# Performance work log

Measured on AMD Instinct MI355X. Metric: run time of the kernel, lower is better.

The kernel has to match this reference:

```python
import jax, jax.numpy as jnp
import numpy as np

B, IN, NC, O, H = 256, 2048, 1000, 4096, 4  # batch, in_features, num_classes, n_decoders, hidden
NEG_SLOPE = 0.1

def setup_inputs() -> dict:
    key = jax.random.key(0)
    ks = jax.random.split(key, 7)
    s1 = 1.0 / np.sqrt(IN)
    s2 = 1.0 / np.sqrt(H)
    return {
        "x":   jax.random.normal(ks[0], (B, IN), jnp.float32),
        "fcW": jax.random.normal(ks[1], (NC, IN), jnp.float32) * s1,
        "fcb": jax.random.normal(ks[2], (NC,), jnp.float32) * s1,
        "W1":  jax.random.normal(ks[3], (O, IN, H), jnp.float32) * s1,
        "b1":  jax.random.normal(ks[4], (O, H), jnp.float32) * s1,
        "W2":  jax.random.normal(ks[5], (O, H), jnp.float32) * s2,
        "b2":  jax.random.normal(ks[6], (O,), jnp.float32) * s2,
    }

def reference(x, fcW, fcb, W1, b1, W2, b2):
    # fc head: x1 = x @ fcW^T + fcb  -> [B, NC]
    x1 = jnp.einsum("bi,ci->bc", x, fcW) + fcb
    # 4096 tiny MLPs batched into one grouped GEMM:
    # h = leaky_relu(x @ W1_o + b1_o) for each decoder o  -> [B, O, H]
    h = jnp.einsum("bi,oih->boh", x, W1) + b1
    h = jnp.where(h >= 0, h, NEG_SLOPE * h)
    # second layer (H->1) collapses to a weighted reduction -> [B, O]
    x2 = jnp.einsum("boh,oh->bo", h, W2) + b2
    return (x1, x2)
```

## Files before the change

kernel.cpp:

```cpp
#include <hip/hip_runtime.h>


typedef __bf16 bf16_t;
typedef __bf16 bf16x8 __attribute__((ext_vector_type(8)));
typedef float  f32x4  __attribute__((ext_vector_type(4)));
typedef float  f32x16 __attribute__((ext_vector_type(16)));

#define GLDS(gp, lp) __builtin_amdgcn_global_load_lds( \
    (const __attribute__((address_space(1))) void*)(gp), \
    (__attribute__((address_space(3))) void*)(lp), 16, 0, 0)

#define WS_A_OFF 0
#define WS_F_OFF (64 * 16384)

__global__ __launch_bounds__(256)
void pack_tiles(const float* __restrict__ x, const float* __restrict__ fcW,
                char* __restrict__ ws)
{
    const int tid = threadIdx.x;
    const int bid = blockIdx.x;
    if (bid < 64) {
        const int rg = bid >> 5, kt = bid & 31;
        char* dst = ws + WS_A_OFF + (size_t)bid * 16384;
        #pragma unroll
        for (int i = 0; i < 4; ++i) {
            const int gi = tid + 256 * i;
            const int r = gi >> 3, s = gi & 7, g = s ^ (r & 7);
            const float* sp = x + (size_t)(rg * 128 + r) * 2048 + kt * 64 + g * 8;
            f32x4 v0 = *(const f32x4*)sp, v1 = *(const f32x4*)(sp + 4);
            bf16x8 o;
            #pragma unroll
            for (int c = 0; c < 4; ++c) { o[c] = (bf16_t)v0[c]; o[4 + c] = (bf16_t)v1[c]; }
            *(bf16x8*)(dst + r * 128 + s * 16) = o;
        }
    } else {
        const int t = bid - 64;
        const int cg = t >> 5, kt = t & 31;
        char* dst = ws + WS_F_OFF + (size_t)t * 8192;
        #pragma unroll
        for (int i = 0; i < 2; ++i) {
            const int gi = tid + 256 * i;
            const int n = gi >> 3, s = gi & 7, g = s ^ (n & 7);
            const int c = cg * 64 + n;
            bf16x8 o;
            if (c < 1000) {
                const float* sp = fcW + (size_t)c * 2048 + kt * 64 + g * 8;
                f32x4 v0 = *(const f32x4*)sp, v1 = *(const f32x4*)(sp + 4);
                #pragma unroll
                for (int cc = 0; cc < 4; ++cc) { o[cc] = (bf16_t)v0[cc]; o[4 + cc] = (bf16_t)v1[cc]; }
            } else {
                #pragma unroll
                for (int cc = 0; cc < 8; ++cc) o[cc] = (bf16_t)0.f;
            }
            *(bf16x8*)(dst + n * 128 + s * 16) = o;
        }
    }
}

__global__ __launch_bounds__(256, 1)
void fused_dual(const char* __restrict__ ws,
                const float* __restrict__ W1,
                const float* __restrict__ fcb,
                const float* __restrict__ b1,
                const float* __restrict__ W2,
                const float* __restrict__ b2,
                float* __restrict__ out)
{
    __shared__ __align__(16) char lds[131072];
    char* lB = lds;

    const int tid  = threadIdx.x;
    const int lane = tid & 63, w = tid >> 6;
    const int l31  = lane & 31, half = lane >> 5;

    const int idx = blockIdx.x;
    const int wid = (idx < 512) ? ((idx & 7) * 64 + (idx >> 3)) : idx;
    const bool is_fc = (wid >= 512);
    const int d   = wid;
    const int fcI = wid - 512;

    const int o_loc = tid & 7;
    const float* w1o = W1 + (size_t)(d * 8 + o_loc) * 8192;
    const int cbase = (tid >> 3) * 4;

    const int cgo = fcI >> 1, rowhalf = fcI & 1;
    const char* fcSrc = ws + WS_F_OFF + (size_t)cgo * 32 * 8192 + rowhalf * 4096;

    f32x4 rga[8], rgb[8];
    auto BL = [&](int kh, int r, f32x4* R) {
        const float* p = w1o + kh * 4096 + (cbase + r) * 32;
        #pragma unroll
        for (int j = 0; j < 8; ++j) R[j] = *(const f32x4*)(p + j * 4);
    };
    auto BW = [&](int r, const f32x4* R) {
        const int idxk = cbase + r;
        const int ktl = idxk >> 3, g = idxk & 7;
        char* base = lB + ktl * 4096 + (4 * o_loc) * 128;
        #pragma unroll
        for (int h = 0; h < 4; ++h) {
            bf16x8 v;
            #pragma unroll
            for (int j = 0; j < 8; ++j) v[j] = (bf16_t)R[j][h];
            const int n7 = (4 * o_loc + h) & 7;
            *(bf16x8*)(base + h * 128 + ((g ^ n7) << 4)) = v;
        }
    };

    auto GLDS_A = [&](int ktg, int pbuf) {
        char* dst = lds + 65536 + pbuf * 32768 + w * 8192;
        const char* src = ws + WS_A_OFF + (size_t)(w >> 1) * 524288
                        + (size_t)ktg * 16384 + (w & 1) * 8192 + lane * 16;
        #pragma unroll
        for (int i = 0; i < 8; ++i)
            GLDS(src + i * 1024, dst + i * 1024);
    };

    f32x16 acc[2];
    #pragma unroll
    for (int i = 0; i < 2; ++i)
        #pragma unroll
        for (int r = 0; r < 16; ++r) acc[i][r] = 0.f;

    for (int kh = 0; kh < 2; ++kh) {
        if (is_fc) {
            #pragma unroll
            for (int ktl = 0; ktl < 16; ++ktl)
                GLDS(fcSrc + (size_t)(kh * 16 + ktl) * 8192 + w * 1024 + lane * 16,
                     lB + ktl * 4096 + w * 1024);
        } else {
            BL(kh, 0, rga); BL(kh, 1, rgb);
            BW(0, rga);     BL(kh, 2, rga);
            BW(1, rgb);     BL(kh, 3, rgb);
            BW(2, rga);     BW(3, rgb);
        }
        GLDS_A(kh * 16, 0);
        __syncthreads();

        for (int ktl = 0; ktl < 16; ++ktl) {
            const int p = ktl & 1;
            if (ktl < 15) GLDS_A(kh * 16 + ktl + 1, p ^ 1);
            const char* A  = lds + 65536 + p * 32768;
            const char* Bt = lB + ktl * 4096;
            #pragma unroll
            for (int ks = 0; ks < 4; ++ks) {
                const int g = ks * 2 + half;
                bf16x8 bf = *(const bf16x8*)(Bt + l31 * 128 + ((g ^ (l31 & 7)) << 4));
                #pragma unroll
                for (int i = 0; i < 2; ++i) {
                    const int mrow = w * 64 + i * 32 + l31;
                    bf16x8 af = *(const bf16x8*)(A + mrow * 128 + ((g ^ (mrow & 7)) << 4));
                    acc[i] = __builtin_amdgcn_mfma_f32_32x32x16_bf16(af, bf, acc[i], 0, 0, 0);
                }
            }
            asm volatile("s_waitcnt vmcnt(0)" ::: "memory");
            __builtin_amdgcn_s_barrier();
            asm volatile("" ::: "memory");
        }
    }

    if (is_fc) {
        const int c = fcI * 32 + l31;
        if (c < 1000) {
            const float bias = fcb[c];
            #pragma unroll
            for (int i = 0; i < 2; ++i)
            #pragma unroll
            for (int r = 0; r < 16; ++r) {
                const int m = w * 64 + i * 32 + (r & 3) + 8 * (r >> 2) + 4 * half;
                out[m * 1000 + c] = acc[i][r] + bias;
            }
        }
    } else {
        float* x2 = out + 256 * 1000;
        const int n_glob = d * 32 + l31;
        const float b1v = b1[n_glob], w2v = W2[n_glob];
        const float b2v = b2[n_glob >> 2];
        float* xs = (float*)(lds + 65536);
        const int o8 = l31 >> 2;
        #pragma unroll
        for (int i = 0; i < 2; ++i)
        #pragma unroll
        for (int r = 0; r < 16; ++r) {
            float h = acc[i][r] + b1v;
            h = (h >= 0.f) ? h : 0.1f * h;
            float wv = h * w2v;
            wv += __shfl_xor(wv, 1, 64);
            wv += __shfl_xor(wv, 2, 64);
            if ((lane & 3) == 0) {
                const int row = w * 64 + i * 32 + (r & 3) + 8 * (r >> 2) + 4 * half;
                xs[row * 8 + o8] = wv + b2v;
            }
        }
        __syncthreads();
        #pragma unroll
        for (int j = 0; j < 2; ++j) {
            const int row = (tid >> 1) + j * 128, part = tid & 1;
            f32x4 v = *(const f32x4*)(xs + row * 8 + part * 4);
            *(f32x4*)(x2 + (size_t)row * 4096 + d * 8 + part * 4) = v;
        }
    }
}

extern "C" void kernel_launch(void* const* d_in, const int* in_sizes, int n_in,
                              void* d_out, int out_size, void* d_ws, size_t ws_size,
                              hipStream_t stream)
{
    (void)in_sizes; (void)n_in; (void)out_size; (void)ws_size;
    const float* x   = (const float*)d_in[0];
    const float* fcW = (const float*)d_in[1];
    const float* fcb = (const float*)d_in[2];
    const float* W1  = (const float*)d_in[3];
    const float* b1  = (const float*)d_in[4];
    const float* W2  = (const float*)d_in[5];
    const float* b2  = (const float*)d_in[6];
    char* ws = (char*)d_ws;
    pack_tiles<<<576, 256, 0, stream>>>(x, fcW, ws);
    fused_dual<<<544, 256, 0, stream>>>(ws, W1, fcb, b1, W2, b2, (float*)d_out);
}
```

Measured before the change: 267.3 us.

## Stream B tiles through small double-buffered LDS and load A fragments directly

The fused kernel no longer stages the whole B panel and A tiles in 128KB of LDS. It streams one 64-wide K slice of B at a time through two 4KB LDS buffers, with loads for the next slice overlapping the current MFMAs. A is pre-packed into MFMA-fragment order, replicated four times in workspace, and read straight into registers, removing the A LDS traffic. fcW is now converted to bf16 inside the main kernel instead of in a separate packing pass. The block mapping is interleaved across 68 groups per XCD-like stride, and launch bounds allow 3 blocks per CU so all 544 blocks can be resident at once. The cost is more per-iteration barriers and global A reads that depend on L2 hits.

```diff
diff --git a/kernel.cpp b/kernel.cpp
--- a/kernel.cpp
+++ b/kernel.cpp
@@ -2,118 +2,89 @@
 
 
 typedef __bf16 bf16_t;
+typedef __bf16 bf16x2v __attribute__((ext_vector_type(2)));
 typedef __bf16 bf16x8 __attribute__((ext_vector_type(8)));
 typedef float  f32x4  __attribute__((ext_vector_type(4)));
 typedef float  f32x16 __attribute__((ext_vector_type(16)));
 
-#define GLDS(gp, lp) __builtin_amdgcn_global_load_lds( \
-    (const __attribute__((address_space(1))) void*)(gp), \
-    (__attribute__((address_space(3))) void*)(lp), 16, 0, 0)
-
-#define WS_A_OFF 0
-#define WS_F_OFF (64 * 16384)
+#define WS_REP_BYTES (1 << 20)
+
+__device__ __forceinline__ int bslot(int n, int g) {
+    return g ^ (n & 7) ^ (((n >> 3) & 3) << 1);
+}
 
 __global__ __launch_bounds__(256)
-void pack_tiles(const float* __restrict__ x, const float* __restrict__ fcW,
-                char* __restrict__ ws)
+void pack_a(const float* __restrict__ x, char* __restrict__ ws)
 {
+    const int kt  = blockIdx.x & 31;
+    const int rep = blockIdx.x >> 5;
+    char* dst = ws + (size_t)rep * WS_REP_BYTES + (size_t)kt * 32768;
     const int tid = threadIdx.x;
-    const int bid = blockIdx.x;
-    if (bid < 64) {
-        const int rg = bid >> 5, kt = bid & 31;
-        char* dst = ws + WS_A_OFF + (size_t)bid * 16384;
-        #pragma unroll
-        for (int i = 0; i < 4; ++i) {
-            const int gi = tid + 256 * i;
-            const int r = gi >> 3, s = gi & 7, g = s ^ (r & 7);
-            const float* sp = x + (size_t)(rg * 128 + r) * 2048 + kt * 64 + g * 8;
-            f32x4 v0 = *(const f32x4*)sp, v1 = *(const f32x4*)(sp + 4);
-            bf16x8 o;
-            #pragma unroll
-            for (int c = 0; c < 4; ++c) { o[c] = (bf16_t)v0[c]; o[4 + c] = (bf16_t)v1[c]; }
-            *(bf16x8*)(dst + r * 128 + s * 16) = o;
-        }
-    } else {
-        const int t = bid - 64;
-        const int cg = t >> 5, kt = t & 31;
-        char* dst = ws + WS_F_OFF + (size_t)t * 8192;
-        #pragma unroll
-        for (int i = 0; i < 2; ++i) {
-            const int gi = tid + 256 * i;
-            const int n = gi >> 3, s = gi & 7, g = s ^ (n & 7);
-            const int c = cg * 64 + n;
-            bf16x8 o;
-            if (c < 1000) {
-                const float* sp = fcW + (size_t)c * 2048 + kt * 64 + g * 8;
-                f32x4 v0 = *(const f32x4*)sp, v1 = *(const f32x4*)(sp + 4);
-                #pragma unroll
-                for (int cc = 0; cc < 4; ++cc) { o[cc] = (bf16_t)v0[cc]; o[4 + cc] = (bf16_t)v1[cc]; }
-            } else {
-                #pragma unroll
-                for (int cc = 0; cc < 8; ++cc) o[cc] = (bf16_t)0.f;
-            }
-            *(bf16x8*)(dst + n * 128 + s * 16) = o;
-        }
-    }
-}
-
-__global__ __launch_bounds__(256, 1)
+    #pragma unroll
+    for (int ii = 0; ii < 8; ++ii) {
+        const int gi  = tid + 256 * ii;
+        const int mr5 = gi >> 8, g = (gi >> 5) & 7, l = gi & 31;
+        const float* sp = x + (size_t)(mr5 * 32 + l) * 2048 + kt * 64 + g * 8;
+        f32x4 v0 = *(const f32x4*)sp, v1 = *(const f32x4*)(sp + 4);
+        bf16x8 o;
+        #pragma unroll
+        for (int c = 0; c < 4; ++c) { o[c] = (bf16_t)v0[c]; o[4 + c] = (bf16_t)v1[c]; }
+        *(bf16x8*)(dst + gi * 16) = o;
+    }
+}
+
+__global__ __launch_bounds__(256, 3)
 void fused_dual(const char* __restrict__ ws,
                 const float* __restrict__ W1,
+                const float* __restrict__ fcW,
                 const float* __restrict__ fcb,
                 const float* __restrict__ b1,
                 const float* __restrict__ W2,
                 const float* __restrict__ b2,
                 float* __restrict__ out)
 {
-    __shared__ __align__(16) char lds[131072];
-    char* lB = lds;
+    __shared__ __align__(16) char lds[2][4096];
 
     const int tid  = threadIdx.x;
     const int lane = tid & 63, w = tid >> 6;
     const int l31  = lane & 31, half = lane >> 5;
 
     const int idx = blockIdx.x;
-    const int wid = (idx < 512) ? ((idx & 7) * 64 + (idx >> 3)) : idx;
+    const int wid = (idx & 7) * 68 + (idx >> 3);
     const bool is_fc = (wid >= 512);
     const int d   = wid;
     const int fcI = wid - 512;
 
-    const int o_loc = tid & 7;
-    const float* w1o = W1 + (size_t)(d * 8 + o_loc) * 8192;
-    const int cbase = (tid >> 3) * 4;
-
-    const int cgo = fcI >> 1, rowhalf = fcI & 1;
-    const char* fcSrc = ws + WS_F_OFF + (size_t)cgo * 32 * 8192 + rowhalf * 4096;
-
-    f32x4 rga[8], rgb[8];
-    auto BL = [&](int kh, int r, f32x4* R) {
-        const float* p = w1o + kh * 4096 + (cbase + r) * 32;
-        #pragma unroll
-        for (int j = 0; j < 8; ++j) R[j] = *(const f32x4*)(p + j * 4);
-    };
-    auto BW = [&](int r, const f32x4* R) {
-        const int idxk = cbase + r;
-        const int ktl = idxk >> 3, g = idxk & 7;
-        char* base = lB + ktl * 4096 + (4 * o_loc) * 128;
+    const char* aRep = ws + (size_t)((idx & 7) >> 1) * WS_REP_BYTES;
+    const int aoff = w * 8192 + half * 512 + l31 * 16;
+
+    const float* bSrc;
+    int bStep;
+    int dwo[4];
+    int fcWoff = 0;
+    if (is_fc) {
+        const int n = tid >> 3, kg = tid & 7;
+        int c = fcI * 32 + n; if (c > 999) c = 999;
+        bSrc = fcW + (size_t)c * 2048 + kg * 8;
+        bStep = 64;
+        fcWoff = n * 128 + bslot(n, kg) * 16;
+        #pragma unroll
+        for (int h = 0; h < 4; ++h) dwo[h] = 0;
+    } else {
+        const int o = (tid >> 5) & 7, kg = (tid >> 2) & 7, kp = tid & 3;
+        bSrc = W1 + (size_t)(d * 8 + o) * 8192 + (kg * 8 + kp * 2) * 4;
+        bStep = 256;
         #pragma unroll
         for (int h = 0; h < 4; ++h) {
-            bf16x8 v;
-            #pragma unroll
-            for (int j = 0; j < 8; ++j) v[j] = (bf16_t)R[j][h];
-            const int n7 = (4 * o_loc + h) & 7;
-            *(bf16x8*)(base + h * 128 + ((g ^ n7) << 4)) = v;
-        }
-    };
-
-    auto GLDS_A = [&](int ktg, int pbuf) {
-        char* dst = lds + 65536 + pbuf * 32768 + w * 8192;
-        const char* src = ws + WS_A_OFF + (size_t)(w >> 1) * 524288
-                        + (size_t)ktg * 16384 + (w & 1) * 8192 + lane * 16;
-        #pragma unroll
-        for (int i = 0; i < 8; ++i)
-            GLDS(src + i * 1024, dst + i * 1024);
-    };
+            const int n = 4 * o + h;
+            dwo[h] = n * 128 + bslot(n, kg) * 16 + kp * 4;
+        }
+    }
+
+    int bro[4];
+    #pragma unroll
+    for (int ks = 0; ks < 4; ++ks)
+        bro[ks] = l31 * 128 + bslot(l31, ks * 2 + half) * 16;
 
     f32x16 acc[2];
     #pragma unroll
@@ -121,38 +92,76 @@
         #pragma unroll
         for (int r = 0; r < 16; ++r) acc[i][r] = 0.f;
 
-    for (int kh = 0; kh < 2; ++kh) {
+    bf16x8 aF0[8], aF1[8];
+    f32x4  bR0[2], bR1[2];
+
+    auto A_PF = [&](int kt, bf16x8* F) {
+        const char* ap = aRep + (size_t)kt * 32768 + aoff;
+        #pragma unroll
+        for (int i = 0; i < 2; ++i)
+            #pragma unroll
+            for (int ks = 0; ks < 4; ++ks)
+                F[i * 4 + ks] = *(const bf16x8*)(ap + i * 4096 + ks * 1024);
+    };
+    auto B_LOAD = [&](int kt, f32x4* R) {
+        const float* p = bSrc + (size_t)kt * bStep;
+        R[0] = *(const f32x4*)p;
+        R[1] = *(const f32x4*)(p + 4);
+    };
+    auto B_WRITE = [&](const f32x4* R, char* lB) {
         if (is_fc) {
-            #pragma unroll
-            for (int ktl = 0; ktl < 16; ++ktl)
-                GLDS(fcSrc + (size_t)(kh * 16 + ktl) * 8192 + w * 1024 + lane * 16,
-                     lB + ktl * 4096 + w * 1024);
+            bf16x8 v;
+            #pragma unroll
+            for (int j = 0; j < 4; ++j) { v[j] = (bf16_t)R[0][j]; v[4 + j] = (bf16_t)R[1][j]; }
+            *(bf16x8*)(lB + fcWoff) = v;
         } else {
-            BL(kh, 0, rga); BL(kh, 1, rgb);
-            BW(0, rga);     BL(kh, 2, rga);
-            BW(1, rgb);     BL(kh, 3, rgb);
-            BW(2, rga);     BW(3, rgb);
-        }
-        GLDS_A(kh * 16, 0);
-        __syncthreads();
-
-        for (int ktl = 0; ktl < 16; ++ktl) {
-            const int p = ktl & 1;
-            if (ktl < 15) GLDS_A(kh * 16 + ktl + 1, p ^ 1);
-            const char* A  = lds + 65536 + p * 32768;
-            const char* Bt = lB + ktl * 4096;
-            #pragma unroll
-            for (int ks = 0; ks < 4; ++ks) {
-                const int g = ks * 2 + half;
-                bf16x8 bf = *(const bf16x8*)(Bt + l31 * 128 + ((g ^ (l31 & 7)) << 4));
-                #pragma unroll
-                for (int i = 0; i < 2; ++i) {
-                    const int mrow = w * 64 + i * 32 + l31;
-                    bf16x8 af = *(const bf16x8*)(A + mrow * 128 + ((g ^ (mrow & 7)) << 4));
-                    acc[i] = __builtin_amdgcn_mfma_f32_32x32x16_bf16(af, bf, acc[i], 0, 0, 0);
-                }
+            #pragma unroll
+            for (int h = 0; h < 4; ++h) {
+                bf16x2v v;
+                v[0] = (bf16_t)R[0][h];
+                v[1] = (bf16_t)R[1][h];
+                *(bf16x2v*)(lB + dwo[h]) = v;
             }
-            asm volatile("s_waitcnt vmcnt(0)" ::: "memory");
+        }
+    };
+    auto MM = [&](const bf16x8* F, const char* lB) {
+        #pragma unroll
+        for (int ks = 0; ks < 4; ++ks) {
+            bf16x8 bf = *(const bf16x8*)(lB + bro[ks]);
+            #pragma unroll
+            for (int i = 0; i < 2; ++i)
+                acc[i] = __builtin_amdgcn_mfma_f32_32x32x16_bf16(F[i * 4 + ks], bf, acc[i], 0, 0, 0);
+        }
+    };
+
+    B_LOAD(0, bR0);
+    B_LOAD(1, bR1);
+    A_PF(0, aF0);
+    B_WRITE(bR0, lds[0]);
+    asm volatile("s_waitcnt lgkmcnt(0)" ::: "memory");
+    __builtin_amdgcn_s_barrier();
+    asm volatile("" ::: "memory");
+
+    for (int t2 = 0; t2 < 16; ++t2) {
+        const int t = t2 * 2;
+        {
+            A_PF(t + 1, aF1);
+            int kb = t + 2; if (kb > 31) kb = 31;
+            B_LOAD(kb, bR0);
+            MM(aF0, lds[0]);
+            B_WRITE(bR1, lds[1]);
+            asm volatile("s_waitcnt lgkmcnt(0)" ::: "memory");
+            __builtin_amdgcn_s_barrier();
+            asm volatile("" ::: "memory");
+        }
+        {
+            int ka = t + 2; if (ka > 31) ka = 31;
+            A_PF(ka, aF0);
+            int kb = t + 3; if (kb > 31) kb = 31;
+            B_LOAD(kb, bR1);
+            MM(aF1, lds[1]);
+            B_WRITE(bR0, lds[0]);
+            asm volatile("s_waitcnt lgkmcnt(0)" ::: "memory");
             __builtin_amdgcn_s_barrier();
             asm volatile("" ::: "memory");
         }
@@ -175,7 +184,7 @@
         const int n_glob = d * 32 + l31;
         const float b1v = b1[n_glob], w2v = W2[n_glob];
         const float b2v = b2[n_glob >> 2];
-        float* xs = (float*)(lds + 65536);
+        float* xs = (float*)lds;
         const int o8 = l31 >> 2;
         #pragma unroll
         for (int i = 0; i < 2; ++i)
@@ -214,6 +223,6 @@
     const float* W2  = (const float*)d_in[5];
     const float* b2  = (const float*)d_in[6];
     char* ws = (char*)d_ws;
-    pack_tiles<<<576, 256, 0, stream>>>(x, fcW, ws);
-    fused_dual<<<544, 256, 0, stream>>>(ws, W1, fcb, b1, W2, b2, (float*)d_out);
-}
+    pack_a<<<128, 256, 0, stream>>>(x, ws);
+    fused_dual<<<544, 256, 0, stream>>>(ws, W1, fcW, fcb, b1, W2, b2, (float*)d_out);
+}
```

Result: faster. 238.2 us (-10.9%).
